# Kernel optimization log

Measured on AMD Instinct MI355X. Metric: run time of the kernel, lower is better.

The kernel has to match this reference:

```python
import math
import jax, jax.numpy as jnp
import numpy as np

EMBED_DIM = 1024
NUM_HEADS = 16
HEAD_DIM = EMBED_DIM // NUM_HEADS


def setup_inputs() -> dict:
    key = jax.random.key(0)
    ks = jax.random.split(key, 10)
    B, S, E = 2, 2048, EMBED_DIM
    x = jax.random.normal(ks[0], (B, S, E), dtype=jnp.float32)
    mask = jax.random.randint(ks[1], (B, S), 0, 2, dtype=jnp.int32)
    s = 1.0 / math.sqrt(E)
    Wq = jax.random.normal(ks[2], (E, E), dtype=jnp.float32) * s
    bq = jnp.zeros((E,), dtype=jnp.float32)
    Wk = jax.random.normal(ks[3], (E, E), dtype=jnp.float32) * s
    bk = jnp.zeros((E,), dtype=jnp.float32)
    Wv = jax.random.normal(ks[4], (E, E), dtype=jnp.float32) * s
    bv = jnp.zeros((E,), dtype=jnp.float32)
    Wo = jax.random.normal(ks[5], (E, E), dtype=jnp.float32) * s
    bo = jnp.zeros((E,), dtype=jnp.float32)
    return {"x": x, "mask": mask, "Wq": Wq, "bq": bq, "Wk": Wk, "bk": bk,
            "Wv": Wv, "bv": bv, "Wo": Wo, "bo": bo}


def reference(x, mask, Wq, bq, Wk, bk, Wv, bv, Wo, bo):
    B, S, E = x.shape
    H, D = NUM_HEADS, HEAD_DIM
    scale = math.sqrt(D)  # ScaledDotProductAttention built with head_dim

    def split_heads(t):
        return t.reshape(B, S, H, D).transpose(0, 2, 1, 3)  # [B,H,S,D]

    q = split_heads(x @ Wq + bq)
    k = split_heads(x @ Wk + bk)
    v = split_heads(x @ Wv + bv)

    scores = jnp.einsum('bhqd,bhkd->bhqk', q, k) / scale  # [B,H,S,S]
    m = mask[:, None, None, :].astype(scores.dtype)        # [B,1,1,S]
    neg = jnp.finfo(scores.dtype).min
    scores = jnp.where(m == 0, neg, scores)
    aw = jax.nn.softmax(scores, axis=-1)
    # post-softmax mask renormalization (as in the torch module)
    aw = aw * m
    denom = aw.sum(axis=-1, keepdims=True)
    aw = jnp.where(denom > 0, aw / jnp.where(denom > 0, denom, 1.0), 0.0)

    ctx = jnp.einsum('bhqk,bhkd->bhqd', aw, v)             # [B,H,S,D]
    ctx = ctx.transpose(0, 2, 1, 3).reshape(B, S, E)
    out = ctx @ Wo + bo
    return out
```

## Files before the change

kernel.cpp:

```cpp
#include <hip/hip_runtime.h>

typedef _Float16 half8 __attribute__((ext_vector_type(8)));
typedef _Float16 half4v __attribute__((ext_vector_type(4)));
typedef _Float16 h2 __attribute__((ext_vector_type(2)));
typedef float f4 __attribute__((ext_vector_type(4)));

#define ASYNC_COPY16(ldsp, gp)                                                     \
  __builtin_amdgcn_global_load_lds((__attribute__((address_space(1))) void*)(gp),  \
                                   (__attribute__((address_space(3))) void*)(ldsp),\
                                   16, 0, 0)

__device__ __forceinline__ f4 mfma16(half8 a, half8 b, f4 c) {
  return __builtin_amdgcn_mfma_f32_16x16x32_f16(a, b, c, 0, 0, 0);
}

__device__ __forceinline__ h2 pack2(float a, float b) {
  return __builtin_bit_cast(h2, __builtin_amdgcn_cvt_pkrtz(a, b));
}

#if defined(__has_builtin)
#if __has_builtin(__builtin_amdgcn_exp2f)
#define EXP2(x) __builtin_amdgcn_exp2f(x)
#endif
#if __has_builtin(__builtin_amdgcn_fdot2)
#define FDOT2(a, b, c) __builtin_amdgcn_fdot2((a), (b), (c), false)
#endif
#endif
#ifndef EXP2
#define EXP2(x) __expf((x) * 0.69314718056f)
#endif
#define KSCALE 0.18033688011f
#define FIXMAX 10.0f


__global__ __launch_bounds__(256) void k_prep(
    const float* __restrict__ x, _Float16* __restrict__ xh,
    const float* __restrict__ Wq, const float* __restrict__ Wk,
    const float* __restrict__ Wv, const float* __restrict__ Wo,
    _Float16* __restrict__ wqkvT, _Float16* __restrict__ woT) {
  __shared__ float tw[32][33];
  const int bid = blockIdx.x, t = threadIdx.x;
  if (bid < 4096) {
    int i = (bid * 256 + t) * 4;
    f4 v = *(const f4*)(x + i);
    half4v h;
    h[0] = (_Float16)v[0]; h[1] = (_Float16)v[1];
    h[2] = (_Float16)v[2]; h[3] = (_Float16)v[3];
    *(half4v*)(xh + i) = h;
    return;
  }
  const int idx = bid - 4096;
  const int z = idx >> 10, rem = idx & 1023;
  const int n0 = (rem & 31) * 32, k0 = (rem >> 5) * 32;
  const float* w = (z == 0) ? Wq : (z == 1) ? Wk : (z == 2) ? Wv : Wo;
  _Float16* wt = (z == 3) ? woT : wqkvT + (size_t)z * 1048576;
  const int tx = t & 31, ty = t >> 5;
  for (int j = 0; j < 32; j += 8) tw[ty + j][tx] = w[(size_t)(k0 + ty + j) * 1024 + n0 + tx];
  __syncthreads();
  for (int j = 0; j < 32; j += 8)
    wt[(size_t)(n0 + ty + j) * 1024 + k0 + tx] = (_Float16)tw[tx][ty + j];
}

__global__ __launch_bounds__(256) void k_gemm_proj(
    const _Float16* __restrict__ A, const _Float16* __restrict__ Bt,
    const float* __restrict__ bq, const float* __restrict__ bk, const float* __restrict__ bv,
    _Float16* __restrict__ Qo, _Float16* __restrict__ Ko, _Float16* __restrict__ Vto) {
  __shared__ __align__(16) _Float16 As[128 * 64];
  __shared__ __align__(16) _Float16 Bs[128 * 64];
  const int t = threadIdx.x, lane = t & 63, w = t >> 6;
  const int qd = lane >> 4, lr = lane & 15;
  const int m0 = blockIdx.y * 128, n0 = blockIdx.x * 128;
  const int wm = (w & 1) * 64, wn = (w >> 1) * 64;
  const f4 z4 = {0.f, 0.f, 0.f, 0.f};
  f4 acc[4][4];
#pragma unroll
  for (int i = 0; i < 4; ++i)
#pragma unroll
    for (int j = 0; j < 4; ++j) acc[i][j] = z4;

  for (int k0 = 0; k0 < 1024; k0 += 64) {
#pragma unroll
    for (int j = 0; j < 4; ++j) {
      int c = t + j * 256;
      int row = c >> 3, col = (c & 7) * 8;
      const _Float16* ga = A + (size_t)(m0 + row) * 1024 + k0 + col;
      const _Float16* gb = Bt + (size_t)(n0 + row) * 1024 + k0 + col;
      char* la = (char*)As + j * 4096 + w * 1024;
      char* lb = (char*)Bs + j * 4096 + w * 1024;
      ASYNC_COPY16(la, ga);
      ASYNC_COPY16(lb, gb);
    }
    __syncthreads();
#pragma unroll
    for (int ks = 0; ks < 2; ++ks) {
      half8 af[4], bf[4];
#pragma unroll
      for (int i = 0; i < 4; ++i)
        af[i] = *(const half8*)(As + (wm + i * 16 + lr) * 64 + ks * 32 + qd * 8);
#pragma unroll
      for (int j = 0; j < 4; ++j)
        bf[j] = *(const half8*)(Bs + (wn + j * 16 + lr) * 64 + ks * 32 + qd * 8);
#pragma unroll
      for (int i = 0; i < 4; ++i)
#pragma unroll
        for (int j = 0; j < 4; ++j) acc[i][j] = mfma16(af[i], bf[j], acc[i][j]);
    }
    __syncthreads();
  }

  const int mat = n0 >> 10;
  const float* bias = (mat == 0) ? bq : (mat == 1) ? bk : bv;
  if (mat == 2) {
#pragma unroll
    for (int i = 0; i < 4; ++i)
#pragma unroll
      for (int j = 0; j < 4; ++j) {
        int n = (n0 + wn + j * 16 + lr) & 1023;
        int hh = n >> 6, d = n & 63;
        int mb = m0 + wm + i * 16 + qd * 4;
        int bb = mb >> 11, sb = mb & 2047;
        float bval = bias[n];
        half4v hv;
#pragma unroll
        for (int r = 0; r < 4; ++r) hv[r] = (_Float16)(acc[i][j][r] + bval);
        *(half4v*)(Vto + ((size_t)(bb * 16 + hh) * 64 + d) * 2048 + sb) = hv;
      }
  } else {
    _Float16* outp = (mat == 0) ? Qo : Ko;
    const float scl = (mat == 0) ? KSCALE : 1.f;
#pragma unroll
    for (int i = 0; i < 4; ++i)
#pragma unroll
      for (int j = 0; j < 4; ++j)
#pragma unroll
        for (int r = 0; r < 4; ++r) {
          int m = m0 + wm + i * 16 + qd * 4 + r;
          int n = (n0 + wn + j * 16 + lr) & 1023;
          float v = (acc[i][j][r] + bias[n]) * scl;
          int bb = m >> 11, s = m & 2047, hh = n >> 6, d = n & 63;
          outp[(size_t)((bb * 16 + hh) * 2048 + s) * 64 + d] = (_Float16)v;
        }
  }
}

__global__ __launch_bounds__(256, 2) void k_attn(
    const _Float16* __restrict__ Qg, const _Float16* __restrict__ Kg,
    const _Float16* __restrict__ Vtg, const int* __restrict__ maskg,
    _Float16* __restrict__ Op, float* __restrict__ ml) {
  __shared__ __align__(16) _Float16 Ks[64][72];
  __shared__ __align__(16) _Float16 Vts[64][72];
  __shared__ __align__(16) _Float16 Pq[4][16][72];
  __shared__ float Msk[64];

  const int bh = blockIdx.y;
  const int b = bh >> 4;
  const int q0 = blockIdx.x * 128;
  const int z = blockIdx.z;
  const int kb = z * 1024;
  const int t = threadIdx.x, lane = t & 63, w = t >> 6;
  const int qd = lane >> 4, lr = lane & 15;

  half8 qf[2][2];
#pragma unroll
  for (int rt = 0; rt < 2; ++rt)
#pragma unroll
    for (int ks = 0; ks < 2; ++ks)
      qf[rt][ks] = *(const half8*)(Qg + (size_t)(bh * 2048 + q0 + w * 32 + rt * 16 + lr) * 64 +
                                   ks * 32 + qd * 8);

  float l_i[2] = {0.f, 0.f};
  const f4 z4 = {0.f, 0.f, 0.f, 0.f};
  f4 O[2][4];
#pragma unroll
  for (int rt = 0; rt < 2; ++rt)
#pragma unroll
    for (int dt = 0; dt < 4; ++dt) O[rt][dt] = z4;

  const int sr0 = t >> 3, scc = (t & 7) * 8;
  const int sr1 = sr0 + 32;
  const _Float16* Kbase = Kg + (size_t)bh * 2048 * 64 + (size_t)kb * 64;
  const _Float16* Vtbase = Vtg + (size_t)bh * 64 * 2048 + kb;

  f4 kr0 = *(const f4*)(Kbase + (size_t)sr0 * 64 + scc);
  f4 kr1 = *(const f4*)(Kbase + (size_t)sr1 * 64 + scc);
  f4 vr0 = *(const f4*)(Vtbase + (size_t)sr0 * 2048 + scc);
  f4 vr1 = *(const f4*)(Vtbase + (size_t)sr1 * 2048 + scc);
  float mval = 0.f;
  if (t < 64) mval = maskg[b * 2048 + kb + t] ? -FIXMAX : -30010.f;

#if defined(FDOT2)
  const h2 one2 = {(_Float16)1.f, (_Float16)1.f};
#endif

  for (int it = 0; it < 16; ++it) {
    __syncthreads();
    *(f4*)&Ks[sr0][scc] = kr0;
    *(f4*)&Ks[sr1][scc] = kr1;
    *(f4*)&Vts[sr0][scc] = vr0;
    *(f4*)&Vts[sr1][scc] = vr1;
    if (t < 64) Msk[t] = mval;
    __syncthreads();

    if (it < 15) {
      int kk = (it + 1) * 64;
      kr0 = *(const f4*)(Kbase + (size_t)(kk + sr0) * 64 + scc);
      kr1 = *(const f4*)(Kbase + (size_t)(kk + sr1) * 64 + scc);
      vr0 = *(const f4*)(Vtbase + (size_t)sr0 * 2048 + kk + scc);
      vr1 = *(const f4*)(Vtbase + (size_t)sr1 * 2048 + kk + scc);
      if (t < 64) mval = maskg[b * 2048 + kb + kk + t] ? -FIXMAX : -30010.f;
    }

    f4 sc[2][4];
#pragma unroll
    for (int kt = 0; kt < 4; ++kt) {
      f4 mv = *(const f4*)&Msk[kt * 16 + qd * 4];
      sc[0][kt] = mv;
      sc[1][kt] = mv;
    }
#pragma unroll
    for (int kt = 0; kt < 4; ++kt) {
      half8 k0 = *(const half8*)&Ks[kt * 16 + lr][qd * 8];
      half8 k1 = *(const half8*)&Ks[kt * 16 + lr][32 + qd * 8];
      sc[0][kt] = mfma16(k0, qf[0][0], sc[0][kt]);
      sc[0][kt] = mfma16(k1, qf[0][1], sc[0][kt]);
      sc[1][kt] = mfma16(k0, qf[1][0], sc[1][kt]);
      sc[1][kt] = mfma16(k1, qf[1][1], sc[1][kt]);
    }

#pragma unroll
    for (int rt = 0; rt < 2; ++rt) {
      float s = 0.f;
#pragma unroll
      for (int kt = 0; kt < 4; ++kt) {
        float p0 = EXP2(sc[rt][kt][0]);
        float p1 = EXP2(sc[rt][kt][1]);
        float p2 = EXP2(sc[rt][kt][2]);
        float p3 = EXP2(sc[rt][kt][3]);
        h2 pa = pack2(p0, p1);
        h2 pb = pack2(p2, p3);
#if defined(FDOT2)
        s = FDOT2(pa, one2, s);
        s = FDOT2(pb, one2, s);
#else
        s += p0 + p1 + p2 + p3;
#endif
        half4v hv;
        hv.lo = pa;
        hv.hi = pb;
        *(half4v*)&Pq[w][lr][kt * 16 + qd * 4] = hv;
      }
      s += __shfl_xor(s, 16, 64);
      s += __shfl_xor(s, 32, 64);
      l_i[rt] += s;

      half8 bp0 = *(const half8*)&Pq[w][lr][qd * 8];
      half8 bp1 = *(const half8*)&Pq[w][lr][32 + qd * 8];
#pragma unroll
      for (int dt = 0; dt < 4; ++dt) {
        half8 va0 = *(const half8*)&Vts[dt * 16 + lr][qd * 8];
        half8 va1 = *(const half8*)&Vts[dt * 16 + lr][32 + qd * 8];
        O[rt][dt] = mfma16(va0, bp0, O[rt][dt]);
        O[rt][dt] = mfma16(va1, bp1, O[rt][dt]);
      }
    }
  }

#pragma unroll
  for (int rt = 0; rt < 2; ++rt) {
    int qrow = q0 + w * 32 + rt * 16 + lr;
    size_t rowi = (size_t)(z * 32 + bh) * 2048 + qrow;
    _Float16* op = Op + rowi * 64;
#pragma unroll
    for (int dt = 0; dt < 4; ++dt) {
      half4v hv;
#pragma unroll
      for (int r = 0; r < 4; ++r) hv[r] = (_Float16)O[rt][dt][r];
      *(half4v*)(op + dt * 16 + qd * 4) = hv;
    }
    if (qd == 0) ml[rowi] = l_i[rt];
  }
}

__global__ __launch_bounds__(256) void k_gemm_out(
    const _Float16* __restrict__ Op, const float* __restrict__ ml,
    const _Float16* __restrict__ Bt, const float* __restrict__ bo,
    float* __restrict__ out) {
  __shared__ __align__(16) _Float16 As[64 * 32];
  __shared__ __align__(16) _Float16 Bs[128 * 32];
  const int t = threadIdx.x, lane = t & 63, w = t >> 6;
  const int qd = lane >> 4, lr = lane & 15;
  const int m0 = blockIdx.y * 64, n0 = blockIdx.x * 128;
  const int wm = (w & 1) * 32, wn = (w >> 1) * 64;
  const f4 z4 = {0.f, 0.f, 0.f, 0.f};
  f4 acc[2][4];
#pragma unroll
  for (int i = 0; i < 2; ++i)
#pragma unroll
    for (int j = 0; j < 4; ++j) acc[i][j] = z4;

  const int arow = t >> 2, acol = (t & 3) * 8;
  const int m = m0 + arow, b = m >> 11, s = m & 2047;
  const int c0 = t, c1 = t + 256;
  for (int k0 = 0; k0 < 1024; k0 += 32) {
    int e = k0 + acol;
    int h = e >> 6, d = e & 63;
    size_t r1 = (size_t)(b * 16 + h) * 2048 + s;
    size_t r2 = r1 + 32 * 2048;
    half8 o1 = *(const half8*)(Op + r1 * 64 + d);
    half8 o2 = *(const half8*)(Op + r2 * 64 + d);
    float L = ml[r1] + ml[r2];
    _Float16 hinv = (_Float16)(1.f / fmaxf(L, 1e-20f));
    const _Float16* gb0 = Bt + (size_t)(n0 + (c0 >> 2)) * 1024 + k0 + (c0 & 3) * 8;
    const _Float16* gb1 = Bt + (size_t)(n0 + (c1 >> 2)) * 1024 + k0 + (c1 & 3) * 8;
    char* lb = (char*)Bs + w * 1024;
    ASYNC_COPY16(lb, gb0);
    ASYNC_COPY16(lb + 4096, gb1);
    half8 a;
#pragma unroll
    for (int j = 0; j < 8; ++j) a[j] = (_Float16)((o1[j] + o2[j]) * hinv);
    *(half8*)(As + arow * 32 + acol) = a;
    __syncthreads();
    half8 af[2], bf[4];
#pragma unroll
    for (int i = 0; i < 2; ++i)
      af[i] = *(const half8*)(As + (wm + i * 16 + lr) * 32 + qd * 8);
#pragma unroll
    for (int j = 0; j < 4; ++j)
      bf[j] = *(const half8*)(Bs + (wn + j * 16 + lr) * 32 + qd * 8);
#pragma unroll
    for (int i = 0; i < 2; ++i)
#pragma unroll
      for (int j = 0; j < 4; ++j) acc[i][j] = mfma16(af[i], bf[j], acc[i][j]);
    __syncthreads();
  }
#pragma unroll
  for (int i = 0; i < 2; ++i)
#pragma unroll
    for (int j = 0; j < 4; ++j)
#pragma unroll
      for (int r = 0; r < 4; ++r) {
        int mm = m0 + wm + i * 16 + qd * 4 + r;
        int n = n0 + wn + j * 16 + lr;
        out[(size_t)mm * 1024 + n] = acc[i][j][r] + bo[n];
      }
}

extern "C" void kernel_launch(void* const* d_in, const int* in_sizes, int n_in,
                              void* d_out, int out_size, void* d_ws, size_t ws_size,
                              hipStream_t stream) {
  const float* x = (const float*)d_in[0];
  const int* mask = (const int*)d_in[1];
  const float* Wq = (const float*)d_in[2];
  const float* bq = (const float*)d_in[3];
  const float* Wk = (const float*)d_in[4];
  const float* bk = (const float*)d_in[5];
  const float* Wv = (const float*)d_in[6];
  const float* bv = (const float*)d_in[7];
  const float* Wo = (const float*)d_in[8];
  const float* bo = (const float*)d_in[9];
  float* out = (float*)d_out;
  char* ws = (char*)d_ws;
  const size_t MB = 1 << 20;

  _Float16* Oph   = (_Float16*)(ws + 0);
  _Float16* xh    = (_Float16*)(ws + 0);
  _Float16* wqkvT = (_Float16*)(ws + 8 * MB);
  _Float16* woT   = (_Float16*)(ws + 16 * MB);
  _Float16* Qh    = (_Float16*)(ws + 18 * MB);
  _Float16* Kh    = (_Float16*)(ws + 26 * MB);
  _Float16* Vth   = (_Float16*)(ws + 34 * MB);
  float*    mlw   = (float*)   (ws + 42 * MB);

  k_prep<<<dim3(8192), dim3(256), 0, stream>>>(x, xh, Wq, Wk, Wv, Wo, wqkvT, woT);
  k_gemm_proj<<<dim3(24, 32), dim3(256), 0, stream>>>(xh, wqkvT, bq, bk, bv, Qh, Kh, Vth);
  k_attn<<<dim3(16, 32, 2), dim3(256), 0, stream>>>(Qh, Kh, Vth, mask, Oph, mlw);
  k_gemm_out<<<dim3(8, 64), dim3(256), 0, stream>>>(Oph, mlw, woT, bo, out);
}
```

Measured before the change: 223.5 us.

## Merge split-K attention partials in last-arriving block and shrink projection GEMM K-tile

The attention kernel now counts finished split-K halves with an atomic counter per query tile. Whichever block arrives second combines both partial outputs and their row sums into a normalized fp16 context, writing it into the Q buffer. The output GEMM then loads that context straight into LDS with async copies, with no per-element combine or reciprocal. Separately, the projection GEMM K-tile drops from 64 to 32, halving its LDS use. Risks are the extra fences and atomics, the reuse of the Q buffer (only safe because each block reads just its own Q rows), and more barriers per K step in the projection.

```diff
diff --git a/kernel.cpp b/kernel.cpp
--- a/kernel.cpp
+++ b/kernel.cpp
@@ -37,10 +37,12 @@
     const float* __restrict__ x, _Float16* __restrict__ xh,
     const float* __restrict__ Wq, const float* __restrict__ Wk,
     const float* __restrict__ Wv, const float* __restrict__ Wo,
-    _Float16* __restrict__ wqkvT, _Float16* __restrict__ woT) {
+    _Float16* __restrict__ wqkvT, _Float16* __restrict__ woT,
+    int* __restrict__ ctr) {
   __shared__ float tw[32][33];
   const int bid = blockIdx.x, t = threadIdx.x;
   if (bid < 4096) {
+    if (bid == 0) { ctr[t] = 0; ctr[t + 256] = 0; }
     int i = (bid * 256 + t) * 4;
     f4 v = *(const f4*)(x + i);
     half4v h;
@@ -65,8 +67,8 @@
     const _Float16* __restrict__ A, const _Float16* __restrict__ Bt,
     const float* __restrict__ bq, const float* __restrict__ bk, const float* __restrict__ bv,
     _Float16* __restrict__ Qo, _Float16* __restrict__ Ko, _Float16* __restrict__ Vto) {
-  __shared__ __align__(16) _Float16 As[128 * 64];
-  __shared__ __align__(16) _Float16 Bs[128 * 64];
+  __shared__ __align__(16) _Float16 As[128 * 32];
+  __shared__ __align__(16) _Float16 Bs[128 * 32];
   const int t = threadIdx.x, lane = t & 63, w = t >> 6;
   const int qd = lane >> 4, lr = lane & 15;
   const int m0 = blockIdx.y * 128, n0 = blockIdx.x * 128;
@@ -78,33 +80,30 @@
 #pragma unroll
     for (int j = 0; j < 4; ++j) acc[i][j] = z4;
 
-  for (int k0 = 0; k0 < 1024; k0 += 64) {
-#pragma unroll
-    for (int j = 0; j < 4; ++j) {
-      int c = t + j * 256;
-      int row = c >> 3, col = (c & 7) * 8;
-      const _Float16* ga = A + (size_t)(m0 + row) * 1024 + k0 + col;
-      const _Float16* gb = Bt + (size_t)(n0 + row) * 1024 + k0 + col;
-      char* la = (char*)As + j * 4096 + w * 1024;
-      char* lb = (char*)Bs + j * 4096 + w * 1024;
-      ASYNC_COPY16(la, ga);
-      ASYNC_COPY16(lb, gb);
-    }
-    __syncthreads();
-#pragma unroll
-    for (int ks = 0; ks < 2; ++ks) {
-      half8 af[4], bf[4];
-#pragma unroll
-      for (int i = 0; i < 4; ++i)
-        af[i] = *(const half8*)(As + (wm + i * 16 + lr) * 64 + ks * 32 + qd * 8);
-#pragma unroll
-      for (int j = 0; j < 4; ++j)
-        bf[j] = *(const half8*)(Bs + (wn + j * 16 + lr) * 64 + ks * 32 + qd * 8);
-#pragma unroll
-      for (int i = 0; i < 4; ++i)
-#pragma unroll
-        for (int j = 0; j < 4; ++j) acc[i][j] = mfma16(af[i], bf[j], acc[i][j]);
-    }
+  const int c0 = t, c1 = t + 256;
+  for (int k0 = 0; k0 < 1024; k0 += 32) {
+    const _Float16* ga0 = A + (size_t)(m0 + (c0 >> 2)) * 1024 + k0 + (c0 & 3) * 8;
+    const _Float16* ga1 = A + (size_t)(m0 + (c1 >> 2)) * 1024 + k0 + (c1 & 3) * 8;
+    const _Float16* gb0 = Bt + (size_t)(n0 + (c0 >> 2)) * 1024 + k0 + (c0 & 3) * 8;
+    const _Float16* gb1 = Bt + (size_t)(n0 + (c1 >> 2)) * 1024 + k0 + (c1 & 3) * 8;
+    char* la = (char*)As + w * 1024;
+    char* lb = (char*)Bs + w * 1024;
+    ASYNC_COPY16(la, ga0);
+    ASYNC_COPY16(la + 4096, ga1);
+    ASYNC_COPY16(lb, gb0);
+    ASYNC_COPY16(lb + 4096, gb1);
+    __syncthreads();
+    half8 af[4], bf[4];
+#pragma unroll
+    for (int i = 0; i < 4; ++i)
+      af[i] = *(const half8*)(As + (wm + i * 16 + lr) * 32 + qd * 8);
+#pragma unroll
+    for (int j = 0; j < 4; ++j)
+      bf[j] = *(const half8*)(Bs + (wn + j * 16 + lr) * 32 + qd * 8);
+#pragma unroll
+    for (int i = 0; i < 4; ++i)
+#pragma unroll
+      for (int j = 0; j < 4; ++j) acc[i][j] = mfma16(af[i], bf[j], acc[i][j]);
     __syncthreads();
   }
 
@@ -146,11 +145,13 @@
 __global__ __launch_bounds__(256, 2) void k_attn(
     const _Float16* __restrict__ Qg, const _Float16* __restrict__ Kg,
     const _Float16* __restrict__ Vtg, const int* __restrict__ maskg,
-    _Float16* __restrict__ Op, float* __restrict__ ml) {
+    _Float16* __restrict__ Op, float* __restrict__ ml,
+    _Float16* __restrict__ ctx, int* __restrict__ ctr) {
   __shared__ __align__(16) _Float16 Ks[64][72];
   __shared__ __align__(16) _Float16 Vts[64][72];
   __shared__ __align__(16) _Float16 Pq[4][16][72];
   __shared__ float Msk[64];
+  __shared__ int lastFlag;
 
   const int bh = blockIdx.y;
   const int b = bh >> 4;
@@ -279,12 +280,38 @@
     }
     if (qd == 0) ml[rowi] = l_i[rt];
   }
+
+  __threadfence();
+  __syncthreads();
+  if (t == 0) lastFlag = (atomicAdd(&ctr[bh * 16 + (q0 >> 7)], 1) == 1) ? 1 : 0;
+  __syncthreads();
+  if (lastFlag) {
+    __threadfence();
+    const int zp = 1 - z;
+#pragma unroll
+    for (int rt = 0; rt < 2; ++rt) {
+      int qrow = q0 + w * 32 + rt * 16 + lr;
+      size_t rowp = (size_t)(zp * 32 + bh) * 2048 + qrow;
+      const _Float16* op = Op + rowp * 64;
+      float lp = ml[rowp];
+      float inv = 1.f / fmaxf(l_i[rt] + lp, 1e-20f);
+      _Float16* cp = ctx + ((size_t)bh * 2048 + qrow) * 64;
+#pragma unroll
+      for (int dt = 0; dt < 4; ++dt) {
+        half4v ov = *(const half4v*)(op + dt * 16 + qd * 4);
+        half4v hv;
+#pragma unroll
+        for (int r = 0; r < 4; ++r)
+          hv[r] = (_Float16)((O[rt][dt][r] + (float)ov[r]) * inv);
+        *(half4v*)(cp + dt * 16 + qd * 4) = hv;
+      }
+    }
+  }
 }
 
 __global__ __launch_bounds__(256) void k_gemm_out(
-    const _Float16* __restrict__ Op, const float* __restrict__ ml,
-    const _Float16* __restrict__ Bt, const float* __restrict__ bo,
-    float* __restrict__ out) {
+    const _Float16* __restrict__ ctx, const _Float16* __restrict__ Bt,
+    const float* __restrict__ bo, float* __restrict__ out) {
   __shared__ __align__(16) _Float16 As[64 * 32];
   __shared__ __align__(16) _Float16 Bs[128 * 32];
   const int t = threadIdx.x, lane = t & 63, w = t >> 6;
@@ -299,26 +326,19 @@
     for (int j = 0; j < 4; ++j) acc[i][j] = z4;
 
   const int arow = t >> 2, acol = (t & 3) * 8;
-  const int m = m0 + arow, b = m >> 11, s = m & 2047;
+  const int m = m0 + arow, bb = m >> 11, s = m & 2047;
   const int c0 = t, c1 = t + 256;
   for (int k0 = 0; k0 < 1024; k0 += 32) {
     int e = k0 + acol;
     int h = e >> 6, d = e & 63;
-    size_t r1 = (size_t)(b * 16 + h) * 2048 + s;
-    size_t r2 = r1 + 32 * 2048;
-    half8 o1 = *(const half8*)(Op + r1 * 64 + d);
-    half8 o2 = *(const half8*)(Op + r2 * 64 + d);
-    float L = ml[r1] + ml[r2];
-    _Float16 hinv = (_Float16)(1.f / fmaxf(L, 1e-20f));
+    const _Float16* ga = ctx + ((size_t)(bb * 16 + h) * 2048 + s) * 64 + d;
     const _Float16* gb0 = Bt + (size_t)(n0 + (c0 >> 2)) * 1024 + k0 + (c0 & 3) * 8;
     const _Float16* gb1 = Bt + (size_t)(n0 + (c1 >> 2)) * 1024 + k0 + (c1 & 3) * 8;
+    char* la = (char*)As + w * 1024;
     char* lb = (char*)Bs + w * 1024;
+    ASYNC_COPY16(la, ga);
     ASYNC_COPY16(lb, gb0);
     ASYNC_COPY16(lb + 4096, gb1);
-    half8 a;
-#pragma unroll
-    for (int j = 0; j < 8; ++j) a[j] = (_Float16)((o1[j] + o2[j]) * hinv);
-    *(half8*)(As + arow * 32 + acol) = a;
     __syncthreads();
     half8 af[2], bf[4];
 #pragma unroll
@@ -370,9 +390,10 @@
   _Float16* Kh    = (_Float16*)(ws + 26 * MB);
   _Float16* Vth   = (_Float16*)(ws + 34 * MB);
   float*    mlw   = (float*)   (ws + 42 * MB);
-
-  k_prep<<<dim3(8192), dim3(256), 0, stream>>>(x, xh, Wq, Wk, Wv, Wo, wqkvT, woT);
+  int*      ctrw  = (int*)     (ws + 42 * MB + 524288);
+
+  k_prep<<<dim3(8192), dim3(256), 0, stream>>>(x, xh, Wq, Wk, Wv, Wo, wqkvT, woT, ctrw);
   k_gemm_proj<<<dim3(24, 32), dim3(256), 0, stream>>>(xh, wqkvT, bq, bk, bv, Qh, Kh, Vth);
-  k_attn<<<dim3(16, 32, 2), dim3(256), 0, stream>>>(Qh, Kh, Vth, mask, Oph, mlw);
-  k_gemm_out<<<dim3(8, 64), dim3(256), 0, stream>>>(Oph, mlw, woT, bo, out);
-}
+  k_attn<<<dim3(16, 32, 2), dim3(256), 0, stream>>>(Qh, Kh, Vth, mask, Oph, mlw, Qh, ctrw);
+  k_gemm_out<<<dim3(8, 64), dim3(256), 0, stream>>>(Qh, woT, bo, out);
+}
```

Result: slower. 394.0 us (+76.3%).
